# Kernel optimization log

Hardware: AMD Instinct MI355X
Metric: run time of the kernel (lower is better)

The kernel has to match this reference:

```python
import jax, jax.numpy as jnp
import numpy as np

N_NODES = 100000


def sage_conv(x, src, dst, W_l, b_l, W_r):
    # PyG SAGEConv (aggr='mean'): out = lin_l(mean_j x_j) + lin_r(x_i)
    msg = x[src]  # [E, d] gather of source-node features
    agg = jax.ops.segment_sum(msg, dst, num_segments=N_NODES)  # [N, d]
    deg = jax.ops.segment_sum(jnp.ones((src.shape[0],), x.dtype), dst,
                              num_segments=N_NODES)
    mean = agg / jnp.clip(deg, 1.0, None)[:, None]
    return mean @ W_l.T + b_l + x @ W_r.T


def setup_inputs() -> dict:
    key = jax.random.key(0)
    ks = jax.random.split(key, 12)
    d_in, d_h, d_out, n_edges = 64, 64, 2, 1200000
    s = 1.0 / np.sqrt(d_h)
    inp = {
        "x": jax.random.normal(ks[0], (N_NODES, d_in), dtype=jnp.float32),
        "edge_index": jax.random.randint(ks[1], (2, n_edges), 0, N_NODES,
                                         dtype=jnp.int64),
        "W_l1": jax.random.uniform(ks[2], (d_h, d_in), jnp.float32, -s, s),
        "b_l1": jax.random.uniform(ks[3], (d_h,), jnp.float32, -s, s),
        "W_r1": jax.random.uniform(ks[4], (d_h, d_in), jnp.float32, -s, s),
        "W_l2": jax.random.uniform(ks[5], (d_h, d_h), jnp.float32, -s, s),
        "b_l2": jax.random.uniform(ks[6], (d_h,), jnp.float32, -s, s),
        "W_r2": jax.random.uniform(ks[7], (d_h, d_h), jnp.float32, -s, s),
        "W_c": jax.random.uniform(ks[8], (d_out, d_h), jnp.float32, -s, s),
        "b_c": jax.random.uniform(ks[9], (d_out,), jnp.float32, -s, s),
    }
    return inp


def reference(x, edge_index, W_l1, b_l1, W_r1, W_l2, b_l2, W_r2, W_c, b_c):
    src, dst = edge_index[0], edge_index[1]
    # layer 1 + relu (dropout is identity in eval mode)
    h = jax.nn.relu(sage_conv(x, src, dst, W_l1, b_l1, W_r1))
    # layer 2 (no relu per forward())
    h = sage_conv(h, src, dst, W_l2, b_l2, W_r2)
    # classifier
    return h @ W_c.T + b_c
```

## Files before the change

### kernel.cpp

```cpp
#include <hip/hip_runtime.h>

#define N_NODES 100000
#define D 64
#define NTILES 3125
#define NBUCK 391
#define NBLK_A 512
#define GCNT_N (NBUCK * NBLK_A)
#define NCHUNK ((GCNT_N + 255) / 256)
#define NTILE_T (N_NODES / 32)
#define TROW 72

typedef __attribute__((ext_vector_type(8))) short short8;
typedef __attribute__((ext_vector_type(16))) float f32x16;
union Pack8 { uint4 u; short8 s; };

__device__ __forceinline__ unsigned f2bf(float f) {
  unsigned u = __float_as_uint(f);
  return (u + 0x7fffu + ((u >> 16) & 1u)) >> 16;
}
#define BF_LO(u) __uint_as_float(((unsigned)(u)) << 16)
#define BF_HI(u) __uint_as_float(((unsigned)(u)) & 0xffff0000u)


__global__ __launch_bounds__(256) void passA_count(const int* __restrict__ dst,
                                                   int* __restrict__ gcnt,
                                                   int nE, int ec) {
  __shared__ int cnt[NBUCK];
  int t = threadIdx.x, blk = blockIdx.x;
  for (int i = t; i < NBUCK; i += 256) cnt[i] = 0;
  __syncthreads();
  int e0 = blk * ec, e1 = min(e0 + ec, nE);
  for (int e = e0 + t; e < e1; e += 256) atomicAdd(&cnt[dst[e] >> 8], 1);
  __syncthreads();
  for (int b = t; b < NBUCK; b += 256) gcnt[b * NBLK_A + blk] = cnt[b];
}

__global__ void gscan_p1(const int* __restrict__ g, int* __restrict__ csum) {
  int t = threadIdx.x, b = blockIdx.x;
  int i = b * 256 + t;
  int v = (i < GCNT_N) ? g[i] : 0;
  for (int off = 32; off; off >>= 1) v += __shfl_down(v, off);
  __shared__ int ws4[4];
  if ((t & 63) == 0) ws4[t >> 6] = v;
  __syncthreads();
  if (t == 0) csum[b] = ws4[0] + ws4[1] + ws4[2] + ws4[3];
}

__global__ void gscan_p2(int* __restrict__ csum, int nB) {
  __shared__ int s[1024];
  int t = threadIdx.x;
  int orig = (t < nB) ? csum[t] : 0;
  s[t] = orig;
  __syncthreads();
  for (int off = 1; off < 1024; off <<= 1) {
    int v = (t >= off) ? s[t - off] : 0;
    __syncthreads();
    s[t] += v;
    __syncthreads();
  }
  if (t < nB) csum[t] = s[t] - orig;
}

__global__ void gscan_p3(int* __restrict__ g, const int* __restrict__ csum) {
  __shared__ int s[256];
  int t = threadIdx.x, b = blockIdx.x;
  int i = b * 256 + t;
  int d = (i < GCNT_N) ? g[i] : 0;
  s[t] = d;
  __syncthreads();
  for (int off = 1; off < 256; off <<= 1) {
    int v = (t >= off) ? s[t - off] : 0;
    __syncthreads();
    s[t] += v;
    __syncthreads();
  }
  if (i < GCNT_N) g[i] = s[t] - d + csum[b];
}

__global__ __launch_bounds__(256) void passC_place(const int* __restrict__ src,
                                                   const int* __restrict__ dst,
                                                   const int* __restrict__ S,
                                                   uint2* __restrict__ pairs,
                                                   int nE, int ec) {
  __shared__ int cur[NBUCK];
  int t = threadIdx.x, blk = blockIdx.x;
  for (int b = t; b < NBUCK; b += 256) cur[b] = S[b * NBLK_A + blk];
  __syncthreads();
  int e0 = blk * ec, e1 = min(e0 + ec, nE);
  for (int e = e0 + t; e < e1; e += 256) {
    int d = dst[e];
    int p = atomicAdd(&cur[d >> 8], 1);
    pairs[p] = make_uint2((unsigned)d, (unsigned)src[e]);
  }
}

__global__ __launch_bounds__(256) void passD_csr(const uint2* __restrict__ pairs,
                                                 const int* __restrict__ S,
                                                 int* __restrict__ rowstart,
                                                 int* __restrict__ degI,
                                                 uint2* __restrict__ srt,
                                                 int nE) {
  __shared__ int lh[256];
  __shared__ int sc[256];
  __shared__ int cur[256];
  int t = threadIdx.x, b = blockIdx.x;
  int base = S[b * NBLK_A];
  int end = (b == NBUCK - 1) ? nE : S[(b + 1) * NBLK_A];
  lh[t] = 0;
  __syncthreads();
  for (int p = base + t; p < end; p += 256) atomicAdd(&lh[pairs[p].x & 255], 1);
  __syncthreads();
  int d = lh[t];
  sc[t] = d;
  __syncthreads();
  for (int off = 1; off < 256; off <<= 1) {
    int v = (t >= off) ? sc[t - off] : 0;
    __syncthreads();
    sc[t] += v;
    __syncthreads();
  }
  int ex = sc[t] - d;
  int node = b * 256 + t;
  if (node < N_NODES) {
    rowstart[node] = base + ex;
    degI[node] = d;
  }
  cur[t] = base + ex;
  __syncthreads();
  for (int p = base + t; p < end; p += 256) {
    uint2 e = pairs[p];
    int slot = atomicAdd(&cur[e.x & 255], 1);
    srt[slot] = e;
  }
}

__global__ void wfold_kernel(const float* __restrict__ Wc,
                             const float* __restrict__ Wl2,
                             const float* __restrict__ Wr2,
                             const float* __restrict__ bl2,
                             const float* __restrict__ bc,
                             float* __restrict__ A2, float* __restrict__ B2,
                             float* __restrict__ bfv) {
  int t = threadIdx.x;
  int c = t >> 6, k = t & 63;
  float sa = 0.f, sb = 0.f;
  for (int j = 0; j < 64; ++j) {
    float w = Wc[c * 64 + j];
    sa = fmaf(w, Wl2[j * 64 + k], sa);
    sb = fmaf(w, Wr2[j * 64 + k], sb);
  }
  A2[c * 64 + k] = sa;
  B2[c * 64 + k] = sb;
  if (t < 2) {
    float s = bc[t];
    for (int j = 0; j < 64; ++j) s = fmaf(Wc[t * 64 + j], bl2[j], s);
    bfv[t] = s;
  }
}

__global__ void wprep_kernel(const float* __restrict__ Wl,
                             const float* __restrict__ Wr,
                             unsigned short* __restrict__ wcat) {
  int i = blockIdx.x * 256 + threadIdx.x;
  if (i < 4096) wcat[i] = (unsigned short)f2bf(Wl[i]);
  else if (i < 8192) wcat[i] = (unsigned short)f2bf(Wr[i - 4096]);
}

__global__ __launch_bounds__(256) void transform_mfma(
    const float* __restrict__ x, const unsigned short* __restrict__ wcat,
    const float* __restrict__ bl, unsigned short* __restrict__ t1,
    unsigned short* __restrict__ r1b) {
  int tid = threadIdx.x, lane = tid & 63;
  int l31 = lane & 31, hi = lane >> 5;

  short8 af[4][4];
#pragma unroll
  for (int jt = 0; jt < 4; ++jt)
#pragma unroll
    for (int kk = 0; kk < 4; ++kk)
      af[jt][kk] = *(const short8*)(wcat + (jt * 32 + l31) * 64 + kk * 16 + 8 * hi);

  const f32x16 Z = {0.f, 0.f, 0.f, 0.f, 0.f, 0.f, 0.f, 0.f,
                    0.f, 0.f, 0.f, 0.f, 0.f, 0.f, 0.f, 0.f};
  const float4* x4 = (const float4*)x;

  int gw = (blockIdx.x * 256 + tid) >> 6;
  int nW = (gridDim.x * 256) >> 6;

  for (int tile = gw; tile < NTILE_T; tile += nW) {
    int node = tile * 32 + l31;
    f32x16 acc[4] = {Z, Z, Z, Z};
#pragma unroll
    for (int kk = 0; kk < 4; ++kk) {
      float4 fa = x4[(size_t)node * 16 + kk * 4 + 2 * hi];
      float4 fb = x4[(size_t)node * 16 + kk * 4 + 2 * hi + 1];
      Pack8 pk;
      pk.u.x = f2bf(fa.x) | (f2bf(fa.y) << 16);
      pk.u.y = f2bf(fa.z) | (f2bf(fa.w) << 16);
      pk.u.z = f2bf(fb.x) | (f2bf(fb.y) << 16);
      pk.u.w = f2bf(fb.z) | (f2bf(fb.w) << 16);
      acc[0] = __builtin_amdgcn_mfma_f32_32x32x16_bf16(af[0][kk], pk.s, acc[0], 0, 0, 0);
      acc[1] = __builtin_amdgcn_mfma_f32_32x32x16_bf16(af[1][kk], pk.s, acc[1], 0, 0, 0);
      acc[2] = __builtin_amdgcn_mfma_f32_32x32x16_bf16(af[2][kk], pk.s, acc[2], 0, 0, 0);
      acc[3] = __builtin_amdgcn_mfma_f32_32x32x16_bf16(af[3][kk], pk.s, acc[3], 0, 0, 0);
    }
#pragma unroll
    for (int jt = 0; jt < 2; ++jt)
#pragma unroll
      for (int rg = 0; rg < 4; ++rg) {
        int j0 = jt * 32 + 8 * rg + 4 * hi;
        uint2 p;
        p.x = f2bf(acc[jt][4 * rg + 0]) | (f2bf(acc[jt][4 * rg + 1]) << 16);
        p.y = f2bf(acc[jt][4 * rg + 2]) | (f2bf(acc[jt][4 * rg + 3]) << 16);
        *(uint2*)(t1 + (size_t)node * 64 + j0) = p;
      }
#pragma unroll
    for (int jt = 2; jt < 4; ++jt)
#pragma unroll
      for (int rg = 0; rg < 4; ++rg) {
        int j0 = (jt - 2) * 32 + 8 * rg + 4 * hi;
        float4 bv = ((const float4*)bl)[j0 >> 2];
        uint2 p;
        p.x = f2bf(acc[jt][4 * rg + 0] + bv.x) |
              (f2bf(acc[jt][4 * rg + 1] + bv.y) << 16);
        p.y = f2bf(acc[jt][4 * rg + 2] + bv.z) |
              (f2bf(acc[jt][4 * rg + 3] + bv.w) << 16);
        *(uint2*)(r1b + (size_t)node * 64 + j0) = p;
      }
  }
}

__global__ __launch_bounds__(256) void tile_g1(
    const uint2* __restrict__ srt, const int* __restrict__ rowstart,
    const unsigned short* __restrict__ t1,
    const unsigned short* __restrict__ r1b, const float* __restrict__ A2,
    const float* __restrict__ B2, float2* __restrict__ g2,
    float2* __restrict__ s2, int nE) {
  __shared__ float pAB[4][64];
  __shared__ unsigned short stg[4][2][16 * TROW];
  int t = threadIdx.x, lane = t & 63, w = t >> 6;
  pAB[t >> 6][t & 63] = (t < 128) ? A2[t] : B2[t - 128];
  __syncthreads();

  int tile = blockIdx.x * 4 + w;
  if (tile >= NTILES) return;
  int base = rowstart[tile * 32];
  int end = (tile == NTILES - 1) ? nE : rowstart[(tile + 1) * 32];
  int l31 = lane & 31, hi = lane >> 5;
  int o = lane >> 3, j8 = lane & 7;
  unsigned short* stA = &stg[w][0][0];
  unsigned short* stB = &stg[w][1][0];

  const f32x16 Z = {0.f, 0.f, 0.f, 0.f, 0.f, 0.f, 0.f, 0.f,
                    0.f, 0.f, 0.f, 0.f, 0.f, 0.f, 0.f, 0.f};
  f32x16 acc0 = Z, acc1 = Z;
  int degc = 0;
  int ng = (end > base) ? ((end - base + 15) >> 4) : 0;

  uint2 prA = make_uint2(0u, 0u), prB = make_uint2(0u, 0u);
  int cntA = 0, cntB = 0;
  uint4 vA0 = make_uint4(0, 0, 0, 0), vA1 = vA0, vB0 = vA0, vB1 = vA0;
  if (ng > 0) {
    prA = srt[min(base + (lane & 15), nE - 1)];
    cntA = min(end - base, 16);
    int s0 = __shfl((int)prA.y, o), s1 = __shfl((int)prA.y, 8 + o);
    vA0 = *(const uint4*)(t1 + (size_t)((o < cntA) ? s0 : 0) * 64 + j8 * 8);
    vA1 = *(const uint4*)(t1 + (size_t)((8 + o < cntA) ? s1 : 0) * 64 + j8 * 8);
  }
  if (ng > 1) {
    int nb = base + 16;
    prB = srt[min(nb + (lane & 15), nE - 1)];
    cntB = min(end - nb, 16);
    int s0 = __shfl((int)prB.y, o), s1 = __shfl((int)prB.y, 8 + o);
    vB0 = *(const uint4*)(t1 + (size_t)((o < cntB) ? s0 : 0) * 64 + j8 * 8);
    vB1 = *(const uint4*)(t1 + (size_t)((8 + o < cntB) ? s1 : 0) * 64 + j8 * 8);
  }

  for (int gg = 0; gg < ng; gg += 2) {
    bool hasB = (gg + 1 < ng);
    *(uint4*)(stA + o * TROW + j8 * 8) = vA0;
    *(uint4*)(stA + (8 + o) * TROW + j8 * 8) = vA1;
    if (hasB) {
      *(uint4*)(stB + o * TROW + j8 * 8) = vB0;
      *(uint4*)(stB + (8 + o) * TROW + j8 * 8) = vB1;
    }
    unsigned amA[8], amB[8];
#pragma unroll
    for (int m = 0; m < 8; ++m) {
      int e = 8 * hi + m;
      int dv = __shfl((int)prA.x, e);
      bool ok = (e < cntA) && ((dv & 31) == l31);
      amA[m] = ok ? 0x3F80u : 0u;
      degc += (amA[m] >> 7) & 1;
    }
    if (hasB) {
#pragma unroll
      for (int m = 0; m < 8; ++m) {
        int e = 8 * hi + m;
        int dv = __shfl((int)prB.x, e);
        bool ok = (e < cntB) && ((dv & 31) == l31);
        amB[m] = ok ? 0x3F80u : 0u;
        degc += (amB[m] >> 7) & 1;
      }
    }
    if (gg + 2 < ng) {
      int nb = base + (gg + 2) * 16;
      prA = srt[min(nb + (lane & 15), nE - 1)];
      cntA = min(end - nb, 16);
      int s0 = __shfl((int)prA.y, o), s1 = __shfl((int)prA.y, 8 + o);
      vA0 = *(const uint4*)(t1 + (size_t)((o < cntA) ? s0 : 0) * 64 + j8 * 8);
      vA1 = *(const uint4*)(t1 + (size_t)((8 + o < cntA) ? s1 : 0) * 64 + j8 * 8);
    }
    if (gg + 3 < ng) {
      int nb = base + (gg + 3) * 16;
      prB = srt[min(nb + (lane & 15), nE - 1)];
      cntB = min(end - nb, 16);
      int s0 = __shfl((int)prB.y, o), s1 = __shfl((int)prB.y, 8 + o);
      vB0 = *(const uint4*)(t1 + (size_t)((o < cntB) ? s0 : 0) * 64 + j8 * 8);
      vB1 = *(const uint4*)(t1 + (size_t)((8 + o < cntB) ? s1 : 0) * 64 + j8 * 8);
    }
    {
      Pack8 I;
      I.u.x = amA[0] | (amA[1] << 16);
      I.u.y = amA[2] | (amA[3] << 16);
      I.u.z = amA[4] | (amA[5] << 16);
      I.u.w = amA[6] | (amA[7] << 16);
      unsigned short b0[8], b1[8];
#pragma unroll
      for (int m = 0; m < 8; ++m) {
        b0[m] = stA[(8 * hi + m) * TROW + l31];
        b1[m] = stA[(8 * hi + m) * TROW + 32 + l31];
      }
      Pack8 F0, F1;
      F0.u.x = b0[0] | ((unsigned)b0[1] << 16);
      F0.u.y = b0[2] | ((unsigned)b0[3] << 16);
      F0.u.z = b0[4] | ((unsigned)b0[5] << 16);
      F0.u.w = b0[6] | ((unsigned)b0[7] << 16);
      F1.u.x = b1[0] | ((unsigned)b1[1] << 16);
      F1.u.y = b1[2] | ((unsigned)b1[3] << 16);
      F1.u.z = b1[4] | ((unsigned)b1[5] << 16);
      F1.u.w = b1[6] | ((unsigned)b1[7] << 16);
      acc0 = __builtin_amdgcn_mfma_f32_32x32x16_bf16(F0.s, I.s, acc0, 0, 0, 0);
      acc1 = __builtin_amdgcn_mfma_f32_32x32x16_bf16(F1.s, I.s, acc1, 0, 0, 0);
    }
    if (hasB) {
      Pack8 I;
      I.u.x = amB[0] | (amB[1] << 16);
      I.u.y = amB[2] | (amB[3] << 16);
      I.u.z = amB[4] | (amB[5] << 16);
      I.u.w = amB[6] | (amB[7] << 16);
      unsigned short b0[8], b1[8];
#pragma unroll
      for (int m = 0; m < 8; ++m) {
        b0[m] = stB[(8 * hi + m) * TROW + l31];
        b1[m] = stB[(8 * hi + m) * TROW + 32 + l31];
      }
      Pack8 F0, F1;
      F0.u.x = b0[0] | ((unsigned)b0[1] << 16);
      F0.u.y = b0[2] | ((unsigned)b0[3] << 16);
      F0.u.z = b0[4] | ((unsigned)b0[5] << 16);
      F0.u.w = b0[6] | ((unsigned)b0[7] << 16);
      F1.u.x = b1[0] | ((unsigned)b1[1] << 16);
      F1.u.y = b1[2] | ((unsigned)b1[3] << 16);
      F1.u.z = b1[4] | ((unsigned)b1[5] << 16);
      F1.u.w = b1[6] | ((unsigned)b1[7] << 16);
      acc0 = __builtin_amdgcn_mfma_f32_32x32x16_bf16(F0.s, I.s, acc0, 0, 0, 0);
      acc1 = __builtin_amdgcn_mfma_f32_32x32x16_bf16(F1.s, I.s, acc1, 0, 0, 0);
    }
  }

  float degf = (float)(degc + __shfl_xor(degc, 32));
  float inv = 1.f / fmaxf(degf, 1.f);
  int node = tile * 32 + l31;
  float d0 = 0.f, d1 = 0.f, d2 = 0.f, d3 = 0.f;
#pragma unroll
  for (int fb = 0; fb < 2; ++fb) {
#pragma unroll
    for (int q4 = 0; q4 < 4; ++q4) {
      int f0 = fb * 32 + q4 * 8 + 4 * hi;
      uint2 rv = *(const uint2*)(r1b + (size_t)node * 64 + f0);
      float bias[4] = {BF_LO(rv.x), BF_HI(rv.x), BF_LO(rv.y), BF_HI(rv.y)};
#pragma unroll
      for (int j = 0; j < 4; ++j) {
        float a = fb ? acc1[q4 * 4 + j] : acc0[q4 * 4 + j];
        float hv = fmaxf(fmaf(a, inv, bias[j]), 0.f);
        int f = f0 + j;
        d0 = fmaf(hv, pAB[0][f], d0);
        d1 = fmaf(hv, pAB[1][f], d1);
        d2 = fmaf(hv, pAB[2][f], d2);
        d3 = fmaf(hv, pAB[3][f], d3);
      }
    }
  }
  d0 += __shfl_xor(d0, 32);
  d1 += __shfl_xor(d1, 32);
  d2 += __shfl_xor(d2, 32);
  d3 += __shfl_xor(d3, 32);
  if (hi == 0) {
    g2[node] = make_float2(d0, d1);
    s2[node] = make_float2(d2, d3);
  }
}

__global__ __launch_bounds__(256) void gather2_kernel(
    const int* __restrict__ rowstart, const int* __restrict__ degI,
    const uint2* __restrict__ srt, const float2* __restrict__ g2,
    const float2* __restrict__ s2, const float* __restrict__ bfv,
    float* __restrict__ out, int nE) {
  int tid = threadIdx.x, lane = tid & 63;
  int q = lane >> 4, l16 = lane & 15;
  float bf0 = bfv[0], bf1 = bfv[1];
  int gq = ((blockIdx.x * 256 + tid) >> 6) * 4 + q;
  int strideN = ((gridDim.x * 256) >> 6) * 4;
  for (int n = gq; n < N_NODES; n += strideN) {
    int rs = rowstart[n], dg = degI[n];
    float s0 = 0.f, s1 = 0.f;
    for (int base = 0; base < dg; base += 16) {
      int e = base + l16;
      int a = (int)srt[min(rs + ((e < dg) ? e : 0), nE - 1)].y;
      float2 v = g2[a];
      float m = (e < dg) ? 1.f : 0.f;
      s0 = fmaf(v.x, m, s0);
      s1 = fmaf(v.y, m, s1);
    }
    s0 += __shfl_xor(s0, 1); s0 += __shfl_xor(s0, 2);
    s0 += __shfl_xor(s0, 4); s0 += __shfl_xor(s0, 8);
    s1 += __shfl_xor(s1, 1); s1 += __shfl_xor(s1, 2);
    s1 += __shfl_xor(s1, 4); s1 += __shfl_xor(s1, 8);
    if (l16 == 0) {
      float inv = 1.f / (float)max(dg, 1);
      float2 sv = s2[n];
      out[(size_t)n * 2 + 0] = fmaf(s0, inv, sv.x) + bf0;
      out[(size_t)n * 2 + 1] = fmaf(s1, inv, sv.y) + bf1;
    }
  }
}

extern "C" void kernel_launch(void* const* d_in, const int* in_sizes, int n_in,
                              void* d_out, int out_size, void* d_ws,
                              size_t ws_size, hipStream_t stream) {
  const float* x   = (const float*)d_in[0];
  const int*   ei  = (const int*)d_in[1];
  const float* Wl1 = (const float*)d_in[2];
  const float* bl1 = (const float*)d_in[3];
  const float* Wr1 = (const float*)d_in[4];
  const float* Wl2 = (const float*)d_in[5];
  const float* bl2 = (const float*)d_in[6];
  const float* Wr2 = (const float*)d_in[7];
  const float* Wc  = (const float*)d_in[8];
  const float* bc  = (const float*)d_in[9];
  float* out = (float*)d_out;

  int nE = in_sizes[1] / 2;
  const int* src = ei;
  const int* dst = ei + nE;

  unsigned short* t1 = (unsigned short*)d_ws;
  uint2* pairs = (uint2*)d_ws;
  uint2* srt = (uint2*)(t1 + (size_t)N_NODES * D);
  unsigned short* r1b = (unsigned short*)(srt + nE);
  float2* g2 = (float2*)(r1b + (size_t)N_NODES * D);
  float2* s2 = g2 + N_NODES;
  float* A2 = (float*)(s2 + N_NODES);
  float* B2 = A2 + 128;
  float* bfv = B2 + 128;
  unsigned short* wcat = (unsigned short*)(bfv + 4);
  int* degI = (int*)(wcat + 8192);
  int* rowstart = degI + N_NODES;
  int* gcnt = rowstart + N_NODES;
  int* csum = gcnt + GCNT_N;

  int ec = (nE + NBLK_A - 1) / NBLK_A;

  passA_count<<<NBLK_A, 256, 0, stream>>>(dst, gcnt, nE, ec);
  gscan_p1<<<NCHUNK, 256, 0, stream>>>(gcnt, csum);
  gscan_p2<<<1, 1024, 0, stream>>>(csum, NCHUNK);
  gscan_p3<<<NCHUNK, 256, 0, stream>>>(gcnt, csum);
  passC_place<<<NBLK_A, 256, 0, stream>>>(src, dst, gcnt, pairs, nE, ec);
  passD_csr<<<NBUCK, 256, 0, stream>>>(pairs, gcnt, rowstart, degI, srt, nE);

  wfold_kernel<<<1, 128, 0, stream>>>(Wc, Wl2, Wr2, bl2, bc, A2, B2, bfv);
  wprep_kernel<<<32, 256, 0, stream>>>(Wl1, Wr1, wcat);
  transform_mfma<<<512, 256, 0, stream>>>(x, wcat, bl1, t1, r1b);

  tile_g1<<<(NTILES + 3) / 4, 256, 0, stream>>>(srt, rowstart, t1, r1b, A2,
                                                B2, g2, s2, nE);
  gather2_kernel<<<512, 256, 0, stream>>>(rowstart, degI, srt, g2, s2, bfv,
                                          out, nE);
}
```

Baseline: 144.5 us.

## Split each tile's edges across four waves and merge the weight-prep kernels

tile_g1 now gives each node tile a whole block, with the tile's edge groups split among four waves. The waves' MFMA accumulators and degree counts are reduced through shared memory, and wave 0 runs the epilogue. This aims to raise parallelism and the number of loads in flight per tile in the latency-bound gather/aggregate, at the cost of extra syncs and an LDS reduction with three idle waves in the epilogue. The two small weight-prep kernels are also fused into one to save a launch.

```diff
diff --git a/kernel.cpp b/kernel.cpp
--- a/kernel.cpp
+++ b/kernel.cpp
@@ -134,36 +134,32 @@
   }
 }
 
-__global__ void wfold_kernel(const float* __restrict__ Wc,
-                             const float* __restrict__ Wl2,
-                             const float* __restrict__ Wr2,
-                             const float* __restrict__ bl2,
-                             const float* __restrict__ bc,
-                             float* __restrict__ A2, float* __restrict__ B2,
-                             float* __restrict__ bfv) {
+__global__ __launch_bounds__(256) void prep_kernel(
+    const float* __restrict__ Wc, const float* __restrict__ Wl2,
+    const float* __restrict__ Wr2, const float* __restrict__ bl2,
+    const float* __restrict__ bc, const float* __restrict__ Wl1,
+    const float* __restrict__ Wr1, float* __restrict__ A2,
+    float* __restrict__ B2, float* __restrict__ bfv,
+    unsigned short* __restrict__ wcat) {
   int t = threadIdx.x;
-  int c = t >> 6, k = t & 63;
-  float sa = 0.f, sb = 0.f;
-  for (int j = 0; j < 64; ++j) {
-    float w = Wc[c * 64 + j];
-    sa = fmaf(w, Wl2[j * 64 + k], sa);
-    sb = fmaf(w, Wr2[j * 64 + k], sb);
-  }
-  A2[c * 64 + k] = sa;
-  B2[c * 64 + k] = sb;
+  for (int i = t; i < 8192; i += 256)
+    wcat[i] = (unsigned short)f2bf((i < 4096) ? Wl1[i] : Wr1[i - 4096]);
+  if (t < 128) {
+    int c = t >> 6, k = t & 63;
+    float sa = 0.f, sb = 0.f;
+    for (int j = 0; j < 64; ++j) {
+      float w = Wc[c * 64 + j];
+      sa = fmaf(w, Wl2[j * 64 + k], sa);
+      sb = fmaf(w, Wr2[j * 64 + k], sb);
+    }
+    A2[c * 64 + k] = sa;
+    B2[c * 64 + k] = sb;
+  }
   if (t < 2) {
     float s = bc[t];
     for (int j = 0; j < 64; ++j) s = fmaf(Wc[t * 64 + j], bl2[j], s);
     bfv[t] = s;
   }
-}
-
-__global__ void wprep_kernel(const float* __restrict__ Wl,
-                             const float* __restrict__ Wr,
-                             unsigned short* __restrict__ wcat) {
-  int i = blockIdx.x * 256 + threadIdx.x;
-  if (i < 4096) wcat[i] = (unsigned short)f2bf(Wl[i]);
-  else if (i < 8192) wcat[i] = (unsigned short)f2bf(Wr[i - 4096]);
 }
 
 __global__ __launch_bounds__(256) void transform_mfma(
@@ -238,12 +234,12 @@
     float2* __restrict__ s2, int nE) {
   __shared__ float pAB[4][64];
   __shared__ unsigned short stg[4][2][16 * TROW];
+  __shared__ int ideg[4][64];
   int t = threadIdx.x, lane = t & 63, w = t >> 6;
   pAB[t >> 6][t & 63] = (t < 128) ? A2[t] : B2[t - 128];
   __syncthreads();
 
-  int tile = blockIdx.x * 4 + w;
-  if (tile >= NTILES) return;
+  int tile = blockIdx.x;
   int base = rowstart[tile * 32];
   int end = (tile == NTILES - 1) ? nE : rowstart[(tile + 1) * 32];
   int l31 = lane & 31, hi = lane >> 5;
@@ -251,26 +247,31 @@
   unsigned short* stA = &stg[w][0][0];
   unsigned short* stB = &stg[w][1][0];
 
+  int ngAll = (end > base) ? ((end - base + 15) >> 4) : 0;
+  int gper = (ngAll + 3) >> 2;
+  int wbase = base + min(w * gper, ngAll) * 16;
+  int wend = min(base + min((w + 1) * gper, ngAll) * 16, end);
+
   const f32x16 Z = {0.f, 0.f, 0.f, 0.f, 0.f, 0.f, 0.f, 0.f,
                     0.f, 0.f, 0.f, 0.f, 0.f, 0.f, 0.f, 0.f};
   f32x16 acc0 = Z, acc1 = Z;
   int degc = 0;
-  int ng = (end > base) ? ((end - base + 15) >> 4) : 0;
+  int ng = (wend > wbase) ? ((wend - wbase + 15) >> 4) : 0;
 
   uint2 prA = make_uint2(0u, 0u), prB = make_uint2(0u, 0u);
   int cntA = 0, cntB = 0;
   uint4 vA0 = make_uint4(0, 0, 0, 0), vA1 = vA0, vB0 = vA0, vB1 = vA0;
   if (ng > 0) {
-    prA = srt[min(base + (lane & 15), nE - 1)];
-    cntA = min(end - base, 16);
+    prA = srt[min(wbase + (lane & 15), nE - 1)];
+    cntA = min(wend - wbase, 16);
     int s0 = __shfl((int)prA.y, o), s1 = __shfl((int)prA.y, 8 + o);
     vA0 = *(const uint4*)(t1 + (size_t)((o < cntA) ? s0 : 0) * 64 + j8 * 8);
     vA1 = *(const uint4*)(t1 + (size_t)((8 + o < cntA) ? s1 : 0) * 64 + j8 * 8);
   }
   if (ng > 1) {
-    int nb = base + 16;
+    int nb = wbase + 16;
     prB = srt[min(nb + (lane & 15), nE - 1)];
-    cntB = min(end - nb, 16);
+    cntB = min(wend - nb, 16);
     int s0 = __shfl((int)prB.y, o), s1 = __shfl((int)prB.y, 8 + o);
     vB0 = *(const uint4*)(t1 + (size_t)((o < cntB) ? s0 : 0) * 64 + j8 * 8);
     vB1 = *(const uint4*)(t1 + (size_t)((8 + o < cntB) ? s1 : 0) * 64 + j8 * 8);
@@ -304,17 +305,17 @@
       }
     }
     if (gg + 2 < ng) {
-      int nb = base + (gg + 2) * 16;
+      int nb = wbase + (gg + 2) * 16;
       prA = srt[min(nb + (lane & 15), nE - 1)];
-      cntA = min(end - nb, 16);
+      cntA = min(wend - nb, 16);
       int s0 = __shfl((int)prA.y, o), s1 = __shfl((int)prA.y, 8 + o);
       vA0 = *(const uint4*)(t1 + (size_t)((o < cntA) ? s0 : 0) * 64 + j8 * 8);
       vA1 = *(const uint4*)(t1 + (size_t)((8 + o < cntA) ? s1 : 0) * 64 + j8 * 8);
     }
     if (gg + 3 < ng) {
-      int nb = base + (gg + 3) * 16;
+      int nb = wbase + (gg + 3) * 16;
       prB = srt[min(nb + (lane & 15), nE - 1)];
-      cntB = min(end - nb, 16);
+      cntB = min(wend - nb, 16);
       int s0 = __shfl((int)prB.y, o), s1 = __shfl((int)prB.y, 8 + o);
       vB0 = *(const uint4*)(t1 + (size_t)((o < cntB) ? s0 : 0) * 64 + j8 * 8);
       vB1 = *(const uint4*)(t1 + (size_t)((8 + o < cntB) ? s1 : 0) * 64 + j8 * 8);
@@ -369,36 +370,61 @@
     }
   }
 
-  float degf = (float)(degc + __shfl_xor(degc, 32));
-  float inv = 1.f / fmaxf(degf, 1.f);
-  int node = tile * 32 + l31;
-  float d0 = 0.f, d1 = 0.f, d2 = 0.f, d3 = 0.f;
-#pragma unroll
-  for (int fb = 0; fb < 2; ++fb) {
-#pragma unroll
-    for (int q4 = 0; q4 < 4; ++q4) {
-      int f0 = fb * 32 + q4 * 8 + 4 * hi;
-      uint2 rv = *(const uint2*)(r1b + (size_t)node * 64 + f0);
-      float bias[4] = {BF_LO(rv.x), BF_HI(rv.x), BF_LO(rv.y), BF_HI(rv.y)};
-#pragma unroll
-      for (int j = 0; j < 4; ++j) {
-        float a = fb ? acc1[q4 * 4 + j] : acc0[q4 * 4 + j];
-        float hv = fmaxf(fmaf(a, inv, bias[j]), 0.f);
-        int f = f0 + j;
-        d0 = fmaf(hv, pAB[0][f], d0);
-        d1 = fmaf(hv, pAB[1][f], d1);
-        d2 = fmaf(hv, pAB[2][f], d2);
-        d3 = fmaf(hv, pAB[3][f], d3);
-      }
-    }
-  }
-  d0 += __shfl_xor(d0, 32);
-  d1 += __shfl_xor(d1, 32);
-  d2 += __shfl_xor(d2, 32);
-  d3 += __shfl_xor(d3, 32);
-  if (hi == 0) {
-    g2[node] = make_float2(d0, d1);
-    s2[node] = make_float2(d2, d3);
+  ideg[w][lane] = degc;
+  __syncthreads();
+  float* red = (float*)&stg[0][0][0];
+  for (int r = 1; r < 4; ++r) {
+    if (w == r) {
+#pragma unroll
+      for (int i = 0; i < 16; ++i) {
+        red[i * 64 + lane] = acc0[i];
+        red[(16 + i) * 64 + lane] = acc1[i];
+      }
+    }
+    __syncthreads();
+    if (w == 0) {
+#pragma unroll
+      for (int i = 0; i < 16; ++i) {
+        acc0[i] += red[i * 64 + lane];
+        acc1[i] += red[(16 + i) * 64 + lane];
+      }
+    }
+    __syncthreads();
+  }
+
+  if (w == 0) {
+    int dtot = ideg[0][lane] + ideg[1][lane] + ideg[2][lane] + ideg[3][lane];
+    float degf = (float)(dtot + __shfl_xor(dtot, 32));
+    float inv = 1.f / fmaxf(degf, 1.f);
+    int node = tile * 32 + l31;
+    float d0 = 0.f, d1 = 0.f, d2 = 0.f, d3 = 0.f;
+#pragma unroll
+    for (int fb = 0; fb < 2; ++fb) {
+#pragma unroll
+      for (int q4 = 0; q4 < 4; ++q4) {
+        int f0 = fb * 32 + q4 * 8 + 4 * hi;
+        uint2 rv = *(const uint2*)(r1b + (size_t)node * 64 + f0);
+        float bias[4] = {BF_LO(rv.x), BF_HI(rv.x), BF_LO(rv.y), BF_HI(rv.y)};
+#pragma unroll
+        for (int j = 0; j < 4; ++j) {
+          float a = fb ? acc1[q4 * 4 + j] : acc0[q4 * 4 + j];
+          float hv = fmaxf(fmaf(a, inv, bias[j]), 0.f);
+          int f = f0 + j;
+          d0 = fmaf(hv, pAB[0][f], d0);
+          d1 = fmaf(hv, pAB[1][f], d1);
+          d2 = fmaf(hv, pAB[2][f], d2);
+          d3 = fmaf(hv, pAB[3][f], d3);
+        }
+      }
+    }
+    d0 += __shfl_xor(d0, 32);
+    d1 += __shfl_xor(d1, 32);
+    d2 += __shfl_xor(d2, 32);
+    d3 += __shfl_xor(d3, 32);
+    if (hi == 0) {
+      g2[node] = make_float2(d0, d1);
+      s2[node] = make_float2(d2, d3);
+    }
   }
 }
 
@@ -479,12 +505,12 @@
   passC_place<<<NBLK_A, 256, 0, stream>>>(src, dst, gcnt, pairs, nE, ec);
   passD_csr<<<NBUCK, 256, 0, stream>>>(pairs, gcnt, rowstart, degI, srt, nE);
 
-  wfold_kernel<<<1, 128, 0, stream>>>(Wc, Wl2, Wr2, bl2, bc, A2, B2, bfv);
-  wprep_kernel<<<32, 256, 0, stream>>>(Wl1, Wr1, wcat);
+  prep_kernel<<<1, 256, 0, stream>>>(Wc, Wl2, Wr2, bl2, bc, Wl1, Wr1, A2, B2,
+                                     bfv, wcat);
   transform_mfma<<<512, 256, 0, stream>>>(x, wcat, bl1, t1, r1b);
 
-  tile_g1<<<(NTILES + 3) / 4, 256, 0, stream>>>(srt, rowstart, t1, r1b, A2,
-                                                B2, g2, s2, nE);
+  tile_g1<<<NTILES, 256, 0, stream>>>(srt, rowstart, t1, r1b, A2, B2, g2, s2,
+                                      nE);
   gather2_kernel<<<512, 256, 0, stream>>>(rowstart, degI, srt, g2, s2, bfv,
                                           out, nE);
 }
```

Result: no change. 143.5 us (-0.7%).
